# Performance work log

Measured on AMD Instinct MI355X. Metric: run time of the kernel, lower is better.

The kernel has to match this reference:

```python
import jax, jax.numpy as jnp
import numpy as np

N_NODES, N_EDGES = 50000, 200000
DN, DE, DG = 256, 256, 128

def setup_inputs() -> dict:
    key = jax.random.key(0)
    ks = jax.random.split(key, 8)
    s = lambda d: 1.0 / np.sqrt(d)
    return {
        "nodes": jax.random.normal(ks[0], (N_NODES, DN), jnp.float32),
        "edges": jax.random.normal(ks[1], (N_EDGES, DE), jnp.float32),
        "globals_": jax.random.normal(ks[2], (DG,), jnp.float32),
        "senders": jax.random.randint(ks[3], (N_EDGES,), 0, N_NODES, jnp.int32),
        "receivers": jax.random.randint(ks[4], (N_EDGES,), 0, N_NODES, jnp.int32),
        "We": jax.random.normal(ks[5], (DE + 2 * DN + DG, DE), jnp.float32) * s(DE + 2 * DN + DG),
        "be": jnp.zeros((DE,), jnp.float32),
        "Wn": jax.random.normal(ks[6], (DE + DN + DG, DN), jnp.float32) * s(DE + DN + DG),
        "bn": jnp.zeros((DN,), jnp.float32),
        "Wg": jax.random.normal(ks[7], (DE + DN + DG, DG), jnp.float32) * s(DE + DN + DG),
        "bg": jnp.zeros((DG,), jnp.float32),
    }

def reference(nodes, edges, globals_, senders, receivers, We, be, Wn, bn, Wg, bg):
    E, N = edges.shape[0], nodes.shape[0]
    # --- edge processor: phi_e([e, v_s, v_r, u]) ---
    edge_in = jnp.concatenate(
        [edges, nodes[senders], nodes[receivers],
         jnp.broadcast_to(globals_, (E, globals_.shape[0]))], axis=-1)  # [E, 896]
    new_edges = jax.nn.relu(edge_in @ We + be)  # [E, DE]
    # --- node processor: phi_v([sum_incoming_e, v, u]) ---
    agg_e = jax.ops.segment_sum(new_edges, receivers, num_segments=N)  # [N, DE]
    node_in = jnp.concatenate(
        [agg_e, nodes, jnp.broadcast_to(globals_, (N, globals_.shape[0]))], axis=-1)
    new_nodes = jax.nn.relu(node_in @ Wn + bn)  # [N, DN]
    # --- global processor: phi_u([sum_e, sum_v, u]) ---
    global_in = jnp.concatenate(
        [new_edges.sum(axis=0), new_nodes.sum(axis=0), globals_], axis=-1)
    new_globals = jax.nn.relu(global_in @ Wg + bg)  # [DG]
    return new_edges, new_nodes, new_globals
```

## Files before the change

### kernel.cpp

```cpp
#include <hip/hip_runtime.h>

#define E_CNT 200000
#define N_CNT 50000
#define CS_PARTS 128

typedef __attribute__((ext_vector_type(8))) unsigned short ushort8;
typedef __attribute__((ext_vector_type(4))) unsigned short us4;
typedef __attribute__((ext_vector_type(4))) float f32x4;
typedef __bf16 bf16x8 __attribute__((ext_vector_type(8)));

static __device__ __forceinline__ unsigned short f2bf(float f) {
  unsigned int u = __builtin_bit_cast(unsigned int, f);
  u += 0x7FFFu + ((u >> 16) & 1u);
  return (unsigned short)(u >> 16);
}
static __device__ __forceinline__ float bf2f(unsigned short u) {
  unsigned int x = ((unsigned int)u) << 16;
  return __builtin_bit_cast(float, x);
}
static __device__ __forceinline__ void pk_add_bf16(unsigned short* a, unsigned int v) {
  asm volatile("global_atomic_pk_add_bf16 %0, %1, off" ::"v"(a), "v"(v) : "memory");
}

__global__ void prep_all(const float* __restrict__ We, const float* __restrict__ be,
                         const float* __restrict__ Wn, const float* __restrict__ bn,
                         const float* __restrict__ g, unsigned short* __restrict__ BpEe,
                         unsigned short* __restrict__ BpPs, unsigned short* __restrict__ BpPr,
                         unsigned short* __restrict__ BpN, float* __restrict__ ce,
                         float* __restrict__ cn) {
  int bid = blockIdx.x;
  if (bid >= 160) {
    int j = threadIdx.x;
    if (bid == 160) {
      float s = be[j];
      for (int k = 0; k < 128; ++k) s += g[k] * We[(size_t)(768 + k) * 256 + j];
      ce[j] = s;
    } else {
      float s = bn[j];
      for (int k = 0; k < 128; ++k) s += g[k] * Wn[(size_t)(512 + k) * 256 + j];
      cn[j] = s;
    }
    return;
  }
  int sub = bid >> 5;
  const float* W;
  unsigned short* Bp;
  bool perm = false;
  if (sub == 0) { W = We;           Bp = BpEe; }
  else if (sub == 1) { W = We + 65536;  Bp = BpPs; }
  else if (sub == 2) { W = We + 131072; Bp = BpPr; }
  else if (sub == 3) { W = Wn;          Bp = BpN; perm = true; }
  else { W = Wn + 65536; Bp = BpN + 65536; }
  int idx = (bid & 31) * 256 + threadIdx.x;
  int lane = idx & 63;
  int t = idx >> 6;
  int F = t & 15;
  int kc = t >> 4;
  int col = F * 16 + (lane & 15);
  int kb = kc * 32 + (lane >> 4) * 8;
  ushort8 v;
#pragma unroll
  for (int j = 0; j < 8; ++j) {
    int r = kb + j;
    if (perm) r = (r & ~63) | ((r & 3) << 4) | ((r >> 2) & 15);
    v[j] = f2bf(W[(size_t)r * 256 + col]);
  }
  *reinterpret_cast<ushort8*>(Bp + (size_t)idx * 8) = v;
}

template <int NSTEPS, int MODE>
__global__ __launch_bounds__(512, 2) void gemm_core(
    const float* __restrict__ A0, const unsigned short* __restrict__ Ab,
    const float* __restrict__ A1, const unsigned short* __restrict__ Bp,
    const unsigned short* __restrict__ BpAlt, const unsigned short* __restrict__ P1,
    const unsigned short* __restrict__ P2, const float* __restrict__ cvec,
    const int* __restrict__ senders, const int* __restrict__ receivers,
    float* __restrict__ outF, unsigned short* __restrict__ outP,
    unsigned short* __restrict__ outPAlt, unsigned short* __restrict__ aggB,
    int nbHalf, int M) {
  __shared__ unsigned short lds[2][128 * 64];

  int bid = blockIdx.x;
  const unsigned short* BpL = Bp;
  unsigned short* outPL = outP;
  if (MODE == 0 && bid >= nbHalf) {
    BpL = BpAlt;
    outPL = outPAlt;
    bid -= nbHalf;
  }

  const int tid = threadIdx.x;
  const int lane = tid & 63;
  const int wave = tid >> 6;
  const int wm = wave >> 2;
  const int wn = wave & 3;
  const int q = lane >> 4;
  const int lr = lane & 15;
  const int row0 = bid * 128;

  const int sr = tid >> 2;
  const int sc = tid & 3;
  int er = row0 + sr;
  if (er > M - 1) er = M - 1;
  const float* fR = (MODE == 2) ? (A1 + (size_t)er * 256) : (A0 + (size_t)er * 256);
  const unsigned short* bR = (MODE == 2) ? (Ab + (size_t)er * 256) : nullptr;

  const int swz = sr & 7;
  const int wbase = sr * 64;
  const int s0 = ((sc * 2) ^ swz) * 8;
  const int s1 = ((sc * 2 + 1) ^ swz) * 8;

  f32x4 acc[4][4] = {};

  if (MODE == 2) {
    const unsigned short* s = bR + sc * 16;
    *reinterpret_cast<ushort8*>(&lds[0][wbase + s0]) = *reinterpret_cast<const ushort8*>(s);
    *reinterpret_cast<ushort8*>(&lds[0][wbase + s1]) = *reinterpret_cast<const ushort8*>(s + 8);
  } else {
    const float4* p4 = reinterpret_cast<const float4*>(fR + sc * 16);
    float fv[16];
    *reinterpret_cast<float4*>(&fv[0]) = p4[0];
    *reinterpret_cast<float4*>(&fv[4]) = p4[1];
    *reinterpret_cast<float4*>(&fv[8]) = p4[2];
    *reinterpret_cast<float4*>(&fv[12]) = p4[3];
    ushort8 w0, w1;
#pragma unroll
    for (int j = 0; j < 8; ++j) {
      w0[j] = f2bf(fv[j]);
      w1[j] = f2bf(fv[8 + j]);
    }
    *reinterpret_cast<ushort8*>(&lds[0][wbase + s0]) = w0;
    *reinterpret_cast<ushort8*>(&lds[0][wbase + s1]) = w1;
  }
  __syncthreads();

#pragma unroll
  for (int ks = 0; ks < NSTEPS; ++ks) {
    const int cc = ks & 1;

    bf16x8 bfr[2][4];
#pragma unroll
    for (int kk = 0; kk < 2; ++kk) {
      const int kc32 = ks * 2 + kk;
#pragma unroll
      for (int fn = 0; fn < 4; ++fn) {
        const int F = wn * 4 + fn;
        bfr[kk][fn] = __builtin_bit_cast(
            bf16x8, *reinterpret_cast<const ushort8*>(
                        BpL + ((size_t)(kc32 * 16 + F) * 64 + lane) * 8));
      }
    }

    float4 nf0, nf1, nf2, nf3;
    ushort8 nb0, nb1;
    const bool nxt_bf = (MODE == 2) && (ks + 1 < 4);
    if (ks + 1 < NSTEPS) {
      if (nxt_bf) {
        const unsigned short* s = bR + (ks + 1) * 64 + sc * 16;
        nb0 = *reinterpret_cast<const ushort8*>(s);
        nb1 = *reinterpret_cast<const ushort8*>(s + 8);
      } else {
        const float* s = fR + ((MODE == 2) ? (ks + 1 - 4) : (ks + 1)) * 64 + sc * 16;
        const float4* p4 = reinterpret_cast<const float4*>(s);
        nf0 = p4[0];
        nf1 = p4[1];
        nf2 = p4[2];
        nf3 = p4[3];
      }
    }

#pragma unroll
    for (int kk = 0; kk < 2; ++kk) {
      bf16x8 a[4];
#pragma unroll
      for (int fm = 0; fm < 4; ++fm) {
        int r = wm * 64 + fm * 16 + lr;
        int slot = (kk * 4 + q) ^ (r & 7);
        a[fm] = __builtin_bit_cast(
            bf16x8, *reinterpret_cast<const ushort8*>(&lds[cc][r * 64 + slot * 8]));
      }
#pragma unroll
      for (int fm = 0; fm < 4; ++fm)
#pragma unroll
        for (int fn = 0; fn < 4; ++fn)
          acc[fm][fn] = __builtin_amdgcn_mfma_f32_16x16x32_bf16(
              a[fm], bfr[kk][fn], acc[fm][fn], 0, 0, 0);
    }

    if (ks + 1 < NSTEPS) {
      ushort8 w0, w1;
      if (nxt_bf) {
        w0 = nb0;
        w1 = nb1;
      } else {
        float fv[16];
        *reinterpret_cast<float4*>(&fv[0]) = nf0;
        *reinterpret_cast<float4*>(&fv[4]) = nf1;
        *reinterpret_cast<float4*>(&fv[8]) = nf2;
        *reinterpret_cast<float4*>(&fv[12]) = nf3;
#pragma unroll
        for (int j = 0; j < 8; ++j) {
          w0[j] = f2bf(fv[j]);
          w1[j] = f2bf(fv[8 + j]);
        }
      }
      *reinterpret_cast<ushort8*>(&lds[cc ^ 1][wbase + s0]) = w0;
      *reinterpret_cast<ushort8*>(&lds[cc ^ 1][wbase + s1]) = w1;
      __syncthreads();
    }
  }

  float bcol[4];
  if (MODE != 0) {
#pragma unroll
    for (int fn = 0; fn < 4; ++fn) bcol[fn] = cvec[wn * 64 + fn * 16 + lr];
  }
#pragma unroll
  for (int fm = 0; fm < 4; ++fm) {
    int rb = row0 + wm * 64 + fm * 16 + q * 4;
#pragma unroll
    for (int i = 0; i < 4; ++i) {
      int gr = rb + i;
      if (gr < M) {
        if (MODE == 0) {
          us4 pv;
#pragma unroll
          for (int fn = 0; fn < 4; ++fn) pv[fn] = f2bf(acc[fm][fn][i]);
          *reinterpret_cast<us4*>(outPL + (size_t)gr * 256 + wn * 64 + lr * 4) = pv;
        } else if (MODE == 1) {
          int snd = senders[gr], rcv = receivers[gr];
          us4 ps = *reinterpret_cast<const us4*>(P1 + (size_t)snd * 256 + wn * 64 + lr * 4);
          us4 pr = *reinterpret_cast<const us4*>(P2 + (size_t)rcv * 256 + wn * 64 + lr * 4);
          float v[4];
#pragma unroll
          for (int fn = 0; fn < 4; ++fn)
            v[fn] = fmaxf(acc[fm][fn][i] + bcol[fn] + bf2f(ps[fn]) + bf2f(pr[fn]), 0.0f);
#pragma unroll
          for (int fn = 0; fn < 4; ++fn)
            __builtin_nontemporal_store(
                v[fn], &outF[(size_t)gr * 256 + wn * 64 + fn * 16 + lr]);
          unsigned int p01 = (unsigned int)f2bf(v[0]) | ((unsigned int)f2bf(v[1]) << 16);
          unsigned int p23 = (unsigned int)f2bf(v[2]) | ((unsigned int)f2bf(v[3]) << 16);
          unsigned short* ap = aggB + (size_t)rcv * 256 + wn * 64 + lr * 4;
          pk_add_bf16(ap, p01);
          pk_add_bf16(ap + 2, p23);
        } else {
#pragma unroll
          for (int fn = 0; fn < 4; ++fn) {
            int col = wn * 64 + fn * 16 + lr;
            outF[(size_t)gr * 256 + col] = fmaxf(acc[fm][fn][i] + bcol[fn], 0.0f);
          }
        }
      }
    }
  }
}

__global__ void colsum_p1(const float* __restrict__ in, float* __restrict__ part, int rows) {
  const int c4 = threadIdx.x & 63;
  const int rg = threadIdx.x >> 6;
  f32x4 s = {0.f, 0.f, 0.f, 0.f};
  for (int r = blockIdx.x * 4 + rg; r < rows; r += CS_PARTS * 4)
    s += *reinterpret_cast<const f32x4*>(in + (size_t)r * 256 + c4 * 4);
  __shared__ f32x4 red[256];
  red[threadIdx.x] = s;
  __syncthreads();
  if (rg == 0) {
    f32x4 r = red[c4] + red[64 + c4] + red[128 + c4] + red[192 + c4];
    *reinterpret_cast<f32x4*>(part + (size_t)blockIdx.x * 256 + c4 * 4) = r;
  }
}
__global__ void colsum_p2(const float* __restrict__ part, float* __restrict__ out) {
  const int c = threadIdx.x;
  float s = 0.f;
  for (int p = 0; p < CS_PARTS; ++p) s += part[(size_t)p * 256 + c];
  out[c] = s;
}
__global__ void colsum_p1b(const unsigned short* __restrict__ in, float* __restrict__ part,
                           int rows) {
  const int c4 = threadIdx.x & 63;
  const int rg = threadIdx.x >> 6;
  f32x4 s = {0.f, 0.f, 0.f, 0.f};
  for (int r = blockIdx.x * 4 + rg; r < rows; r += CS_PARTS * 4) {
    us4 v = *reinterpret_cast<const us4*>(in + (size_t)r * 256 + c4 * 4);
#pragma unroll
    for (int j = 0; j < 4; ++j) s[j] += bf2f(v[j]);
  }
  __shared__ f32x4 red[256];
  red[threadIdx.x] = s;
  __syncthreads();
  if (rg == 0) {
    f32x4 r = red[c4] + red[64 + c4] + red[128 + c4] + red[192 + c4];
    *reinterpret_cast<f32x4*>(part + (size_t)blockIdx.x * 256 + c4 * 4) = r;
  }
}
__global__ void colsum_p2b(const float* __restrict__ part, float* __restrict__ out) {
  const int s = threadIdx.x;
  float v = 0.f;
  for (int p = 0; p < CS_PARTS; ++p) v += part[(size_t)p * 256 + s];
  int orig = (s & 192) | ((s & 3) << 4) | ((s >> 2) & 15);
  out[orig] = v;
}

__global__ void global_mlp(const float* __restrict__ esum, const float* __restrict__ nsum,
                           const float* __restrict__ gl, const float* __restrict__ Wg,
                           const float* __restrict__ bg, float* __restrict__ out2) {
  __shared__ float red[512];
  int g = threadIdx.x & 127;
  int kg = threadIdx.x >> 7;
  float acc = 0.f;
  for (int k = kg; k < 640; k += 4) {
    float x = (k < 256) ? esum[k] : (k < 512 ? nsum[k - 256] : gl[k - 512]);
    acc += x * Wg[(size_t)k * 128 + g];
  }
  red[threadIdx.x] = acc;
  __syncthreads();
  if (kg == 0) {
    float r = red[g] + red[128 + g] + red[256 + g] + red[384 + g] + bg[g];
    out2[g] = fmaxf(r, 0.f);
  }
}

extern "C" void kernel_launch(void* const* d_in, const int* in_sizes, int n_in,
                              void* d_out, int out_size, void* d_ws, size_t ws_size,
                              hipStream_t stream) {
  const float* nodes = (const float*)d_in[0];
  const float* edges = (const float*)d_in[1];
  const float* gl = (const float*)d_in[2];
  const int* senders = (const int*)d_in[3];
  const int* receivers = (const int*)d_in[4];
  const float* We = (const float*)d_in[5];
  const float* be = (const float*)d_in[6];
  const float* Wn = (const float*)d_in[7];
  const float* bn = (const float*)d_in[8];
  const float* Wg = (const float*)d_in[9];
  const float* bg = (const float*)d_in[10];

  float* out0 = (float*)d_out;
  float* out1 = out0 + (size_t)E_CNT * 256;
  float* out2 = out1 + (size_t)N_CNT * 256;

  char* ws = (char*)d_ws;
  size_t o = 0;
  unsigned short* Ps = (unsigned short*)(ws + o);   o += (size_t)N_CNT * 256 * 2;
  unsigned short* Pr = (unsigned short*)(ws + o);   o += (size_t)N_CNT * 256 * 2;
  unsigned short* aggB = (unsigned short*)(ws + o); o += (size_t)N_CNT * 256 * 2;
  unsigned short* BpEe = (unsigned short*)(ws + o); o += 131072;
  unsigned short* BpPs = (unsigned short*)(ws + o); o += 131072;
  unsigned short* BpPr = (unsigned short*)(ws + o); o += 131072;
  unsigned short* BpN = (unsigned short*)(ws + o);  o += 262144;
  float* ce = (float*)(ws + o);                     o += 1024;
  float* cn = (float*)(ws + o);                     o += 1024;
  float* esum = (float*)(ws + o);                   o += 1024;
  float* nsum = (float*)(ws + o);                   o += 1024;
  float* partE = (float*)(ws + o);                  o += CS_PARTS * 256 * 4;
  float* partN = (float*)(ws + o);                  o += CS_PARTS * 256 * 4;

  hipMemsetAsync(aggB, 0, (size_t)N_CNT * 256 * 2, stream);

  prep_all<<<162, 256, 0, stream>>>(We, be, Wn, bn, gl, BpEe, BpPs, BpPr, BpN, ce, cn);

  const int nbN = (N_CNT + 127) / 128;
  gemm_core<4, 0><<<2 * nbN, 512, 0, stream>>>(
      nodes, nullptr, nullptr, BpPs, BpPr, nullptr, nullptr, nullptr, nullptr,
      nullptr, nullptr, Ps, Pr, nullptr, nbN, N_CNT);

  gemm_core<4, 1><<<(E_CNT + 127) / 128, 512, 0, stream>>>(
      edges, nullptr, nullptr, BpEe, nullptr, Ps, Pr, ce, senders, receivers,
      out0, nullptr, nullptr, aggB, 1 << 30, E_CNT);

  colsum_p1b<<<CS_PARTS, 256, 0, stream>>>(aggB, partE, N_CNT);
  colsum_p2b<<<1, 256, 0, stream>>>(partE, esum);

  gemm_core<8, 2><<<nbN, 512, 0, stream>>>(
      nullptr, aggB, nodes, BpN, nullptr, nullptr, nullptr, cn, nullptr, nullptr,
      out1, nullptr, nullptr, nullptr, 1 << 30, N_CNT);

  colsum_p1<<<CS_PARTS, 256, 0, stream>>>(out1, partN, N_CNT);
  colsum_p2<<<1, 256, 0, stream>>>(partN, nsum);

  global_mlp<<<1, 512, 0, stream>>>(esum, nsum, gl, Wg, bg, out2);
}
```

Before: 449.9 us.

## Sort edges by receiver, aggregate in fp32 with run-merged atomics, fuse column sums

Adds a counting sort of edges by receiver (histogram, scan, scatter) so the edge GEMM processes receiver-sorted rows. Consecutive edges with the same receiver are merged in registers before fp32 atomic adds into a buffer that aliases the node output. This replaces the bf16 packed atomics and the permuted layout. Column sums for the edge and node outputs are fused into the GEMM epilogues via LDS and partial atomics, which removes the separate colsum pass kernels. The cost is extra sort kernels, a single-block scan, gathered edge-row loads and scattered output writes, and fp32 atomics that double the aggregation traffic. The node GEMM now reads fp32 aggregates as the A-matrix input, and the aggregates now carry fp32 rather than bf16 precision.

```diff
diff --git a/kernel.cpp b/kernel.cpp
--- a/kernel.cpp
+++ b/kernel.cpp
@@ -17,9 +17,6 @@
 static __device__ __forceinline__ float bf2f(unsigned short u) {
   unsigned int x = ((unsigned int)u) << 16;
   return __builtin_bit_cast(float, x);
-}
-static __device__ __forceinline__ void pk_add_bf16(unsigned short* a, unsigned int v) {
-  asm volatile("global_atomic_pk_add_bf16 %0, %1, off" ::"v"(a), "v"(v) : "memory");
 }
 
 __global__ void prep_all(const float* __restrict__ We, const float* __restrict__ be,
@@ -45,12 +42,11 @@
   int sub = bid >> 5;
   const float* W;
   unsigned short* Bp;
-  bool perm = false;
-  if (sub == 0) { W = We;           Bp = BpEe; }
-  else if (sub == 1) { W = We + 65536;  Bp = BpPs; }
-  else if (sub == 2) { W = We + 131072; Bp = BpPr; }
-  else if (sub == 3) { W = Wn;          Bp = BpN; perm = true; }
-  else { W = Wn + 65536; Bp = BpN + 65536; }
+  if (sub == 0)      { W = We;           Bp = BpEe; }
+  else if (sub == 1) { W = We + 65536;   Bp = BpPs; }
+  else if (sub == 2) { W = We + 131072;  Bp = BpPr; }
+  else if (sub == 3) { W = Wn;           Bp = BpN; }
+  else               { W = Wn + 65536;   Bp = BpN + 65536; }
   int idx = (bid & 31) * 256 + threadIdx.x;
   int lane = idx & 63;
   int t = idx >> 6;
@@ -60,24 +56,70 @@
   int kb = kc * 32 + (lane >> 4) * 8;
   ushort8 v;
 #pragma unroll
-  for (int j = 0; j < 8; ++j) {
-    int r = kb + j;
-    if (perm) r = (r & ~63) | ((r & 3) << 4) | ((r >> 2) & 15);
-    v[j] = f2bf(W[(size_t)r * 256 + col]);
-  }
+  for (int j = 0; j < 8; ++j) v[j] = f2bf(W[(size_t)(kb + j) * 256 + col]);
   *reinterpret_cast<ushort8*>(Bp + (size_t)idx * 8) = v;
+}
+
+__global__ void hist(const int* __restrict__ recv, int* __restrict__ count) {
+  int e = blockIdx.x * blockDim.x + threadIdx.x;
+  if (e < E_CNT) atomicAdd(&count[recv[e]], 1);
+}
+
+__global__ __launch_bounds__(1024) void scan_build(const int* __restrict__ count,
+                                                   int* __restrict__ offs,
+                                                   int* __restrict__ cursor) {
+  __shared__ int part[1024];
+  const int t = threadIdx.x;
+  const int CH = 49;
+  const int base = t * CH;
+  int s = 0;
+  for (int i = 0; i < CH; ++i) {
+    int idx = base + i;
+    if (idx < N_CNT) s += count[idx];
+  }
+  part[t] = s;
+  __syncthreads();
+  for (int d = 1; d < 1024; d <<= 1) {
+    int v = (t >= d) ? part[t - d] : 0;
+    __syncthreads();
+    part[t] += v;
+    __syncthreads();
+  }
+  int run = (t == 0) ? 0 : part[t - 1];
+  for (int i = 0; i < CH; ++i) {
+    int idx = base + i;
+    if (idx < N_CNT) {
+      offs[idx] = run;
+      cursor[idx] = run;
+      run += count[idx];
+    }
+  }
+  if (t == 1023) offs[N_CNT] = run;
+}
+
+__global__ void scatter(const int* __restrict__ recv, const int* __restrict__ snd,
+                        int* __restrict__ cursor, int* __restrict__ eord,
+                        int* __restrict__ sndS, int* __restrict__ rcvS) {
+  int e = blockIdx.x * blockDim.x + threadIdx.x;
+  if (e < E_CNT) {
+    int r = recv[e];
+    int pos = atomicAdd(&cursor[r], 1);
+    eord[pos] = e;
+    rcvS[pos] = r;
+    sndS[pos] = snd[e];
+  }
 }
 
 template <int NSTEPS, int MODE>
 __global__ __launch_bounds__(512, 2) void gemm_core(
-    const float* __restrict__ A0, const unsigned short* __restrict__ Ab,
-    const float* __restrict__ A1, const unsigned short* __restrict__ Bp,
-    const unsigned short* __restrict__ BpAlt, const unsigned short* __restrict__ P1,
-    const unsigned short* __restrict__ P2, const float* __restrict__ cvec,
-    const int* __restrict__ senders, const int* __restrict__ receivers,
+    const float* __restrict__ A0, const float* __restrict__ A1,
+    const unsigned short* __restrict__ Bp, const unsigned short* __restrict__ BpAlt,
+    const unsigned short* __restrict__ P1, const unsigned short* __restrict__ P2,
+    const float* __restrict__ cvec, const int* __restrict__ eord,
+    const int* __restrict__ sndS, const int* __restrict__ rcvS,
     float* __restrict__ outF, unsigned short* __restrict__ outP,
-    unsigned short* __restrict__ outPAlt, unsigned short* __restrict__ aggB,
-    int nbHalf, int M) {
+    unsigned short* __restrict__ outPAlt, float* __restrict__ agg,
+    float* __restrict__ part, int nbHalf, int M) {
   __shared__ unsigned short lds[2][128 * 64];
 
   int bid = blockIdx.x;
@@ -102,8 +144,11 @@
   const int sc = tid & 3;
   int er = row0 + sr;
   if (er > M - 1) er = M - 1;
-  const float* fR = (MODE == 2) ? (A1 + (size_t)er * 256) : (A0 + (size_t)er * 256);
-  const unsigned short* bR = (MODE == 2) ? (Ab + (size_t)er * 256) : nullptr;
+  int srow = er;
+  if (MODE == 1) srow = eord[er];
+  const float* sbase[2];
+  sbase[0] = A0 + (size_t)srow * 256;
+  sbase[1] = (MODE == 2) ? (A1 + (size_t)srow * 256) : sbase[0];
 
   const int swz = sr & 7;
   const int wbase = sr * 64;
@@ -112,12 +157,8 @@
 
   f32x4 acc[4][4] = {};
 
-  if (MODE == 2) {
-    const unsigned short* s = bR + sc * 16;
-    *reinterpret_cast<ushort8*>(&lds[0][wbase + s0]) = *reinterpret_cast<const ushort8*>(s);
-    *reinterpret_cast<ushort8*>(&lds[0][wbase + s1]) = *reinterpret_cast<const ushort8*>(s + 8);
-  } else {
-    const float4* p4 = reinterpret_cast<const float4*>(fR + sc * 16);
+  {
+    const float4* p4 = reinterpret_cast<const float4*>(sbase[0] + sc * 16);
     float fv[16];
     *reinterpret_cast<float4*>(&fv[0]) = p4[0];
     *reinterpret_cast<float4*>(&fv[4]) = p4[1];
@@ -152,21 +193,13 @@
     }
 
     float4 nf0, nf1, nf2, nf3;
-    ushort8 nb0, nb1;
-    const bool nxt_bf = (MODE == 2) && (ks + 1 < 4);
     if (ks + 1 < NSTEPS) {
-      if (nxt_bf) {
-        const unsigned short* s = bR + (ks + 1) * 64 + sc * 16;
-        nb0 = *reinterpret_cast<const ushort8*>(s);
-        nb1 = *reinterpret_cast<const ushort8*>(s + 8);
-      } else {
-        const float* s = fR + ((MODE == 2) ? (ks + 1 - 4) : (ks + 1)) * 64 + sc * 16;
-        const float4* p4 = reinterpret_cast<const float4*>(s);
-        nf0 = p4[0];
-        nf1 = p4[1];
-        nf2 = p4[2];
-        nf3 = p4[3];
-      }
+      const float4* p4 = reinterpret_cast<const float4*>(
+          sbase[(ks + 1) >> 2] + ((ks + 1) & 3) * 64 + sc * 16);
+      nf0 = p4[0];
+      nf1 = p4[1];
+      nf2 = p4[2];
+      nf3 = p4[3];
     }
 
 #pragma unroll
@@ -188,21 +221,16 @@
     }
 
     if (ks + 1 < NSTEPS) {
+      float fv[16];
+      *reinterpret_cast<float4*>(&fv[0]) = nf0;
+      *reinterpret_cast<float4*>(&fv[4]) = nf1;
+      *reinterpret_cast<float4*>(&fv[8]) = nf2;
+      *reinterpret_cast<float4*>(&fv[12]) = nf3;
       ushort8 w0, w1;
-      if (nxt_bf) {
-        w0 = nb0;
-        w1 = nb1;
-      } else {
-        float fv[16];
-        *reinterpret_cast<float4*>(&fv[0]) = nf0;
-        *reinterpret_cast<float4*>(&fv[4]) = nf1;
-        *reinterpret_cast<float4*>(&fv[8]) = nf2;
-        *reinterpret_cast<float4*>(&fv[12]) = nf3;
-#pragma unroll
-        for (int j = 0; j < 8; ++j) {
-          w0[j] = f2bf(fv[j]);
-          w1[j] = f2bf(fv[8 + j]);
-        }
+#pragma unroll
+      for (int j = 0; j < 8; ++j) {
+        w0[j] = f2bf(fv[j]);
+        w1[j] = f2bf(fv[8 + j]);
       }
       *reinterpret_cast<ushort8*>(&lds[cc ^ 1][wbase + s0]) = w0;
       *reinterpret_cast<ushort8*>(&lds[cc ^ 1][wbase + s1]) = w1;
@@ -215,91 +243,96 @@
 #pragma unroll
     for (int fn = 0; fn < 4; ++fn) bcol[fn] = cvec[wn * 64 + fn * 16 + lr];
   }
+  float cs[4] = {0.f, 0.f, 0.f, 0.f};
+
 #pragma unroll
   for (int fm = 0; fm < 4; ++fm) {
     int rb = row0 + wm * 64 + fm * 16 + q * 4;
-#pragma unroll
-    for (int i = 0; i < 4; ++i) {
-      int gr = rb + i;
-      if (gr < M) {
-        if (MODE == 0) {
+    if (MODE == 0) {
+#pragma unroll
+      for (int i = 0; i < 4; ++i) {
+        int gr = rb + i;
+        if (gr < M) {
           us4 pv;
 #pragma unroll
           for (int fn = 0; fn < 4; ++fn) pv[fn] = f2bf(acc[fm][fn][i]);
           *reinterpret_cast<us4*>(outPL + (size_t)gr * 256 + wn * 64 + lr * 4) = pv;
-        } else if (MODE == 1) {
-          int snd = senders[gr], rcv = receivers[gr];
+        }
+      }
+    } else if (MODE == 1) {
+      float runv[4];
+      int runr = -1;
+#pragma unroll
+      for (int i = 0; i < 4; ++i) {
+        int gr = rb + i;
+        if (gr < M) {
+          int e = eord[gr];
+          int snd = sndS[gr];
+          int rcv = rcvS[gr];
           us4 ps = *reinterpret_cast<const us4*>(P1 + (size_t)snd * 256 + wn * 64 + lr * 4);
           us4 pr = *reinterpret_cast<const us4*>(P2 + (size_t)rcv * 256 + wn * 64 + lr * 4);
           float v[4];
 #pragma unroll
-          for (int fn = 0; fn < 4; ++fn)
+          for (int fn = 0; fn < 4; ++fn) {
             v[fn] = fmaxf(acc[fm][fn][i] + bcol[fn] + bf2f(ps[fn]) + bf2f(pr[fn]), 0.0f);
-#pragma unroll
-          for (int fn = 0; fn < 4; ++fn)
+            cs[fn] += v[fn];
             __builtin_nontemporal_store(
-                v[fn], &outF[(size_t)gr * 256 + wn * 64 + fn * 16 + lr]);
-          unsigned int p01 = (unsigned int)f2bf(v[0]) | ((unsigned int)f2bf(v[1]) << 16);
-          unsigned int p23 = (unsigned int)f2bf(v[2]) | ((unsigned int)f2bf(v[3]) << 16);
-          unsigned short* ap = aggB + (size_t)rcv * 256 + wn * 64 + lr * 4;
-          pk_add_bf16(ap, p01);
-          pk_add_bf16(ap + 2, p23);
-        } else {
-#pragma unroll
-          for (int fn = 0; fn < 4; ++fn) {
-            int col = wn * 64 + fn * 16 + lr;
-            outF[(size_t)gr * 256 + col] = fmaxf(acc[fm][fn][i] + bcol[fn], 0.0f);
+                v[fn], &outF[(size_t)e * 256 + wn * 64 + fn * 16 + lr]);
+          }
+          if (rcv == runr) {
+#pragma unroll
+            for (int fn = 0; fn < 4; ++fn) runv[fn] += v[fn];
+          } else {
+            if (runr >= 0) {
+#pragma unroll
+              for (int fn = 0; fn < 4; ++fn)
+                atomicAdd(agg + (size_t)runr * 256 + wn * 64 + fn * 16 + lr, runv[fn]);
+            }
+            runr = rcv;
+#pragma unroll
+            for (int fn = 0; fn < 4; ++fn) runv[fn] = v[fn];
           }
         }
       }
-    }
-  }
-}
-
-__global__ void colsum_p1(const float* __restrict__ in, float* __restrict__ part, int rows) {
-  const int c4 = threadIdx.x & 63;
-  const int rg = threadIdx.x >> 6;
-  f32x4 s = {0.f, 0.f, 0.f, 0.f};
-  for (int r = blockIdx.x * 4 + rg; r < rows; r += CS_PARTS * 4)
-    s += *reinterpret_cast<const f32x4*>(in + (size_t)r * 256 + c4 * 4);
-  __shared__ f32x4 red[256];
-  red[threadIdx.x] = s;
-  __syncthreads();
-  if (rg == 0) {
-    f32x4 r = red[c4] + red[64 + c4] + red[128 + c4] + red[192 + c4];
-    *reinterpret_cast<f32x4*>(part + (size_t)blockIdx.x * 256 + c4 * 4) = r;
-  }
-}
+      if (runr >= 0) {
+#pragma unroll
+        for (int fn = 0; fn < 4; ++fn)
+          atomicAdd(agg + (size_t)runr * 256 + wn * 64 + fn * 16 + lr, runv[fn]);
+      }
+    } else {
+#pragma unroll
+      for (int i = 0; i < 4; ++i) {
+        int gr = rb + i;
+        if (gr < M) {
+#pragma unroll
+          for (int fn = 0; fn < 4; ++fn) {
+            float v = fmaxf(acc[fm][fn][i] + bcol[fn], 0.0f);
+            cs[fn] += v;
+            outF[(size_t)gr * 256 + wn * 64 + fn * 16 + lr] = v;
+          }
+        }
+      }
+    }
+  }
+
+  if (MODE != 0) {
+    float* csum = reinterpret_cast<float*>(&lds[0][0]);
+    __syncthreads();
+    if (tid < 256) csum[tid] = 0.f;
+    __syncthreads();
+#pragma unroll
+    for (int fn = 0; fn < 4; ++fn) atomicAdd(&csum[wn * 64 + fn * 16 + lr], cs[fn]);
+    __syncthreads();
+    if (tid < 256)
+      atomicAdd(&part[(size_t)(blockIdx.x & (CS_PARTS - 1)) * 256 + tid], csum[tid]);
+  }
+}
+
 __global__ void colsum_p2(const float* __restrict__ part, float* __restrict__ out) {
   const int c = threadIdx.x;
   float s = 0.f;
   for (int p = 0; p < CS_PARTS; ++p) s += part[(size_t)p * 256 + c];
   out[c] = s;
-}
-__global__ void colsum_p1b(const unsigned short* __restrict__ in, float* __restrict__ part,
-                           int rows) {
-  const int c4 = threadIdx.x & 63;
-  const int rg = threadIdx.x >> 6;
-  f32x4 s = {0.f, 0.f, 0.f, 0.f};
-  for (int r = blockIdx.x * 4 + rg; r < rows; r += CS_PARTS * 4) {
-    us4 v = *reinterpret_cast<const us4*>(in + (size_t)r * 256 + c4 * 4);
-#pragma unroll
-    for (int j = 0; j < 4; ++j) s[j] += bf2f(v[j]);
-  }
-  __shared__ f32x4 red[256];
-  red[threadIdx.x] = s;
-  __syncthreads();
-  if (rg == 0) {
-    f32x4 r = red[c4] + red[64 + c4] + red[128 + c4] + red[192 + c4];
-    *reinterpret_cast<f32x4*>(part + (size_t)blockIdx.x * 256 + c4 * 4) = r;
-  }
-}
-__global__ void colsum_p2b(const float* __restrict__ part, float* __restrict__ out) {
-  const int s = threadIdx.x;
-  float v = 0.f;
-  for (int p = 0; p < CS_PARTS; ++p) v += part[(size_t)p * 256 + s];
-  int orig = (s & 192) | ((s & 3) << 4) | ((s >> 2) & 15);
-  out[orig] = v;
 }
 
 __global__ void global_mlp(const float* __restrict__ esum, const float* __restrict__ nsum,
@@ -340,11 +373,21 @@
   float* out1 = out0 + (size_t)E_CNT * 256;
   float* out2 = out1 + (size_t)N_CNT * 256;
 
+  float* agg = out1;
+
   char* ws = (char*)d_ws;
   size_t o = 0;
+  int* count = (int*)(ws + o);                      o += 200704;
+  float* partE = (float*)(ws + o);                  o += CS_PARTS * 256 * 4;
+  float* partN = (float*)(ws + o);                  o += CS_PARTS * 256 * 4;
+  size_t zeroBytes = o;
+  int* offs = (int*)(ws + o);                       o += 200704;
+  int* cursor = (int*)(ws + o);                     o += 200704;
+  int* eord = (int*)(ws + o);                       o += 800000;
+  int* sndS = (int*)(ws + o);                       o += 800000;
+  int* rcvS = (int*)(ws + o);                       o += 800000;
   unsigned short* Ps = (unsigned short*)(ws + o);   o += (size_t)N_CNT * 256 * 2;
   unsigned short* Pr = (unsigned short*)(ws + o);   o += (size_t)N_CNT * 256 * 2;
-  unsigned short* aggB = (unsigned short*)(ws + o); o += (size_t)N_CNT * 256 * 2;
   unsigned short* BpEe = (unsigned short*)(ws + o); o += 131072;
   unsigned short* BpPs = (unsigned short*)(ws + o); o += 131072;
   unsigned short* BpPr = (unsigned short*)(ws + o); o += 131072;
@@ -353,30 +396,33 @@
   float* cn = (float*)(ws + o);                     o += 1024;
   float* esum = (float*)(ws + o);                   o += 1024;
   float* nsum = (float*)(ws + o);                   o += 1024;
-  float* partE = (float*)(ws + o);                  o += CS_PARTS * 256 * 4;
-  float* partN = (float*)(ws + o);                  o += CS_PARTS * 256 * 4;
-
-  hipMemsetAsync(aggB, 0, (size_t)N_CNT * 256 * 2, stream);
+
+  hipMemsetAsync(ws, 0, zeroBytes, stream);
+  hipMemsetAsync(agg, 0, (size_t)N_CNT * 256 * 4, stream);
 
   prep_all<<<162, 256, 0, stream>>>(We, be, Wn, bn, gl, BpEe, BpPs, BpPr, BpN, ce, cn);
+
+  hist<<<(E_CNT + 255) / 256, 256, 0, stream>>>(receivers, count);
 
   const int nbN = (N_CNT + 127) / 128;
   gemm_core<4, 0><<<2 * nbN, 512, 0, stream>>>(
-      nodes, nullptr, nullptr, BpPs, BpPr, nullptr, nullptr, nullptr, nullptr,
-      nullptr, nullptr, Ps, Pr, nullptr, nbN, N_CNT);
+      nodes, nullptr, BpPs, BpPr, nullptr, nullptr, nullptr, nullptr, nullptr,
+      nullptr, nullptr, Ps, Pr, nullptr, nullptr, nbN, N_CNT);
+
+  scan_build<<<1, 1024, 0, stream>>>(count, offs, cursor);
+  scatter<<<(E_CNT + 255) / 256, 256, 0, stream>>>(receivers, senders, cursor,
+                                                   eord, sndS, rcvS);
 
   gemm_core<4, 1><<<(E_CNT + 127) / 128, 512, 0, stream>>>(
-      edges, nullptr, nullptr, BpEe, nullptr, Ps, Pr, ce, senders, receivers,
-      out0, nullptr, nullptr, aggB, 1 << 30, E_CNT);
-
-  colsum_p1b<<<CS_PARTS, 256, 0, stream>>>(aggB, partE, N_CNT);
-  colsum_p2b<<<1, 256, 0, stream>>>(partE, esum);
+      edges, nullptr, BpEe, nullptr, Ps, Pr, ce, eord, sndS, rcvS, out0,
+      nullptr, nullptr, agg, partE, 1 << 30, E_CNT);
+
+  colsum_p2<<<1, 256, 0, stream>>>(partE, esum);
 
   gemm_core<8, 2><<<nbN, 512, 0, stream>>>(
-      nullptr, aggB, nodes, BpN, nullptr, nullptr, nullptr, cn, nullptr, nullptr,
-      out1, nullptr, nullptr, nullptr, 1 << 30, N_CNT);
-
-  colsum_p1<<<CS_PARTS, 256, 0, stream>>>(out1, partN, N_CNT);
+      agg, nodes, BpN, nullptr, nullptr, nullptr, cn, nullptr, nullptr, nullptr,
+      out1, nullptr, nullptr, nullptr, partN, 1 << 30, N_CNT);
+
   colsum_p2<<<1, 256, 0, stream>>>(partN, nsum);
 
   global_mlp<<<1, 512, 0, stream>>>(esum, nsum, gl, Wg, bg, out2);
```

New measurement: 543.7 us. 1.21x slower.
